# Performance work log

Measured on AMD Instinct MI355X. Metric: run time of the kernel, lower is better.

## Reference

```python
import jax, jax.numpy as jnp
import numpy as np

B, T, DIM = 4, 2048, 2048
H = 16
Q_LORA, KV_LORA = 1536, 512
ROPE_D, NOPE_D, V_D = 64, 128, 128
Q_HEAD_D = NOPE_D + ROPE_D  # 192
EPS = 1e-6
ROPE_THETA = 500000.0


def rmsnorm(x, w):
    xf = x.astype(jnp.float32)
    rms = jax.lax.rsqrt(jnp.mean(xf * xf, axis=-1, keepdims=True) + EPS)
    return (xf * rms).astype(x.dtype) * w


def apply_rope(x, cos, sin):
    # x: (B,T,H,d); cos/sin: (T,d//2). Complex mult on interleaved pairs.
    d = x.shape[-1]
    xp = x.reshape(*x.shape[:-1], d // 2, 2)
    x0, x1 = xp[..., 0], xp[..., 1]
    c = cos[None, :, None, :]
    s = sin[None, :, None, :]
    o0 = x0 * c - x1 * s
    o1 = x0 * s + x1 * c
    return jnp.stack([o0, o1], axis=-1).reshape(x.shape)


def setup_inputs() -> dict:
    key = jax.random.key(0)
    ks = jax.random.split(key, 8)
    x = jax.random.normal(ks[0], (B, T, DIM), dtype=jnp.float32)
    # RoPE freqs as in standard precompute_freqs_cis
    inv_freq = 1.0 / (ROPE_THETA ** (np.arange(0, ROPE_D, 2, dtype=np.float32) / ROPE_D))
    t = np.arange(T, dtype=np.float32)
    ang = np.outer(t, inv_freq)  # (T, 32)
    freqs_cos = jnp.asarray(np.cos(ang))
    freqs_sin = jnp.asarray(np.sin(ang))
    # causal additive mask (1,1,T,T)
    mask = jnp.where(jnp.tril(jnp.ones((T, T), dtype=bool)), 0.0, -1e9).astype(jnp.float32)[None, None]
    sc = lambda fan_in: 1.0 / np.sqrt(fan_in)
    q_down_w = jax.random.normal(ks[1], (Q_LORA, DIM), dtype=jnp.float32) * sc(DIM)
    q_norm_w = jnp.ones((Q_LORA,), dtype=jnp.float32)
    q_up_nope_w = jax.random.normal(ks[2], (H * NOPE_D, Q_LORA), dtype=jnp.float32) * sc(Q_LORA)
    q_up_rope_w = jax.random.normal(ks[3], (H * ROPE_D, Q_LORA), dtype=jnp.float32) * sc(Q_LORA)
    kv_down_w = jax.random.normal(ks[4], (KV_LORA + ROPE_D, DIM), dtype=jnp.float32) * sc(DIM)
    kv_norm_w = jnp.ones((KV_LORA,), dtype=jnp.float32)
    kv_up_w = jax.random.normal(ks[5], (H * (NOPE_D + V_D), KV_LORA), dtype=jnp.float32) * sc(KV_LORA)
    wo_w = jax.random.normal(ks[6], (DIM, H * V_D), dtype=jnp.float32) * sc(H * V_D)
    return {"x": x, "freqs_cos": freqs_cos, "freqs_sin": freqs_sin, "mask": mask,
            "q_down_w": q_down_w, "q_norm_w": q_norm_w, "q_up_nope_w": q_up_nope_w,
            "q_up_rope_w": q_up_rope_w, "kv_down_w": kv_down_w, "kv_norm_w": kv_norm_w,
            "kv_up_w": kv_up_w, "wo_w": wo_w}


def reference(x, freqs_cos, freqs_sin, mask, q_down_w, q_norm_w, q_up_nope_w,
              q_up_rope_w, kv_down_w, kv_norm_w, kv_up_w, wo_w):
    b, t, _ = x.shape
    # Q path: low-rank down -> RMSNorm -> nope/rope up projections
    c_q = rmsnorm(x @ q_down_w.T, q_norm_w)                      # (B,T,q_lora)
    q_nope = (c_q @ q_up_nope_w.T).reshape(b, t, H, NOPE_D)
    q_rope = (c_q @ q_up_rope_w.T).reshape(b, t, H, ROPE_D)
    q_rope = apply_rope(q_rope, freqs_cos, freqs_sin)
    q = jnp.concatenate([q_nope, q_rope], axis=-1)               # (B,T,H,192)
    # KV path: shared low-rank latent + per-sequence rope key
    kv_raw = x @ kv_down_w.T                                     # (B,T,512+64)
    c_kv = kv_raw[..., :KV_LORA]
    k_rope = kv_raw[..., KV_LORA:][:, :, None, :]                # (B,T,1,64)
    k_rope = apply_rope(k_rope, freqs_cos, freqs_sin)
    k_rope = jnp.broadcast_to(k_rope, (b, t, H, ROPE_D))
    kv = (rmsnorm(c_kv, kv_norm_w) @ kv_up_w.T).reshape(b, t, H, NOPE_D + V_D)
    k_nope = kv[..., :NOPE_D]
    v = kv[..., NOPE_D:]                                         # (B,T,H,128)
    k = jnp.concatenate([k_nope, k_rope], axis=-1)               # (B,T,H,192)
    scale = Q_HEAD_D ** -0.5
    attn = jnp.einsum('bthd,bshd->bhts', q, k) * scale + mask    # (B,H,T,T)
    attn = jax.nn.softmax(attn, axis=-1)
    out = jnp.einsum('bhts,bshd->bthd', attn, v).reshape(b, t, H * V_D)
    return out @ wo_w.T
```

## Files before the change

kernel.cpp:

```cpp
#include <hip/hip_runtime.h>

#define BB 4
#define TT 2048
#define HH 16
#define ROWS (BB*TT)

typedef unsigned short u16;
typedef __bf16 bf16x8 __attribute__((ext_vector_type(8)));
typedef float f32x4 __attribute__((ext_vector_type(4)));
typedef u16 u16x8 __attribute__((ext_vector_type(8)));
typedef u16 u16x4 __attribute__((ext_vector_type(4)));

__device__ __forceinline__ u16 f2bf(float f) {
  unsigned u = __float_as_uint(f);
  u += 0x7fffu + ((u >> 16) & 1u);
  return (u16)(u >> 16);
}
__device__ __forceinline__ float bf2f(u16 h) {
  return __uint_as_float(((unsigned)h) << 16);
}

__device__ __forceinline__ void gload_lds16(const u16* g, u16* l) {
  __builtin_amdgcn_global_load_lds((const __attribute__((address_space(1))) void*)g,
                                   (__attribute__((address_space(3))) void*)l, 16, 0, 0);
}

__global__ __launch_bounds__(256) void cast_all(const float* __restrict__ x,
                                                const float* __restrict__ qdw,
                                                const float* __restrict__ kvdw,
                                                const float* __restrict__ qunw,
                                                const float* __restrict__ qurw,
                                                const float* __restrict__ kvuw,
                                                const float* __restrict__ wow,
                                                u16* __restrict__ xb,
                                                u16* __restrict__ wdc,
                                                u16* __restrict__ wuc,
                                                u16* __restrict__ wkvu,
                                                u16* __restrict__ wwo,
                                                float qsc) {
  const long s0 = 1536L*2048, s1 = 768L*2048, s2 = 2048L*1536,
             s3 = 1024L*1536, s4 = 4096L*512,  s5 = 2048L*2048,
             s6 = (long)ROWS*2048;
  const long total = s0+s1+s2+s3+s4+s5+s6;
  long i = ((long)blockIdx.x * 256 + threadIdx.x) * 4;
  long stride = (long)gridDim.x * 1024;
  for (; i < total; i += stride) {
    long off = i; const float* src; u16* dst; float sc = 1.f; long lim = -1;
    if (off < s0)               { src = qdw;  dst = wdc; }
    else if ((off -= s0) < s1)  { src = kvdw; dst = wdc + s0; lim = 576L*2048; }
    else if ((off -= s1) < s2)  { src = qunw; dst = wuc; sc = qsc; }
    else if ((off -= s2) < s3)  { src = qurw; dst = wuc + s2; }
    else if ((off -= s3) < s4)  { src = kvuw; dst = wkvu; }
    else if ((off -= s4) < s5)  { src = wow;  dst = wwo; }
    else { off -= s5;             src = x;    dst = xb; }
    u16x4 o;
    if (lim < 0 || off + 3 < lim) {
      float4 v = *(const float4*)(src + off);
      o = (u16x4){ f2bf(v.x*sc), f2bf(v.y*sc), f2bf(v.z*sc), f2bf(v.w*sc) };
    } else {
#pragma unroll
      for (int e = 0; e < 4; ++e) o[e] = (off + e < lim) ? f2bf(src[off+e]*sc) : (u16)0;
    }
    *(u16x4*)(dst + off) = o;
  }
}


template<int MODE>
__global__ __launch_bounds__(512, 2) void gemm256(const u16* __restrict__ A,
                                                  const u16* __restrict__ Bm,
                                                  void* __restrict__ Cv,
                                                  int M, int N, int K, int lda) {
  __shared__ __align__(16) u16 lds[32768];
  const int tid = threadIdx.x;
  const int lane = tid & 63, wid = tid >> 6;
  const int wm = (wid >> 2) * 128;
  const int wn = (wid & 3) * 64;

  const int nx = gridDim.x;
  int id = blockIdx.y * nx + blockIdx.x;
  const int cpx = (nx * gridDim.y) >> 3;
  id = (id & 7) * cpx + (id >> 3);
  const int m0 = (id / nx) * 256;
  const int n0 = (id % nx) * 256;

  const int NT = K >> 5;

  f32x4 acc[8][4] = {};

  auto stage = [&](int kt, int d) {
#pragma unroll
    for (int j = 0; j < 2; ++j) {
      int c = j*512 + tid;
      int row = c >> 2;
      int colb = (c & 3) << 4;
      int srcb = colb ^ (((row >> 1) & 3) << 4);
      const u16* ga = (const u16*)((const char*)A + ((long)(m0 + row) * lda + kt*32) * 2 + srcb);
      gload_lds16(ga, (u16*)((char*)lds + d*32768 + c*16));
      const u16* gb = (const u16*)((const char*)Bm + ((long)(n0 + row) * K + kt*32) * 2 + srcb);
      gload_lds16(gb, (u16*)((char*)lds + d*32768 + 16384 + c*16));
    }
  };

  stage(0, 0);
  stage(1, 1);

  const int lr = lane & 15;
  const int kb = (lane >> 4) << 4;

  for (int kt = 0; kt < NT; ++kt) {
    const int cur = kt & 1;
    if (kt + 1 < NT) asm volatile("s_waitcnt vmcnt(4)" ::: "memory");
    else             asm volatile("s_waitcnt vmcnt(0)" ::: "memory");
    __builtin_amdgcn_s_barrier();
    __builtin_amdgcn_sched_barrier(0);

    const char* Ab = (const char*)lds + cur*32768;
    const char* Bb = Ab + 16384;
    bf16x8 af[8], bf[4];
#pragma unroll
    for (int i = 0; i < 8; ++i) {
      int r = wm + i*16 + lr;
      af[i] = *(const bf16x8*)(Ab + r*64 + (kb ^ (((r >> 1) & 3) << 4)));
    }
#pragma unroll
    for (int i = 0; i < 4; ++i) {
      int r = wn + i*16 + lr;
      bf[i] = *(const bf16x8*)(Bb + r*64 + (kb ^ (((r >> 1) & 3) << 4)));
    }
    __builtin_amdgcn_s_setprio(1);
#pragma unroll
    for (int i = 0; i < 8; ++i)
#pragma unroll
      for (int j = 0; j < 4; ++j)
        acc[i][j] = __builtin_amdgcn_mfma_f32_16x16x32_bf16(af[i], bf[j], acc[i][j], 0, 0, 0);
    __builtin_amdgcn_s_setprio(0);
    __builtin_amdgcn_sched_barrier(0);
    __builtin_amdgcn_s_barrier();
    if (kt + 2 < NT) stage(kt + 2, cur);
  }

  const int orow = (lane >> 4) << 2;
  const int ocol = lane & 15;
#pragma unroll
  for (int mf = 0; mf < 8; ++mf)
#pragma unroll
    for (int nf = 0; nf < 4; ++nf) {
      long rbase = (long)(m0 + wm + mf*16 + orow);
      int col = n0 + wn + nf*16 + ocol;
      if (MODE == 0) {
#pragma unroll
        for (int rr = 0; rr < 4; ++rr)
          ((float*)Cv)[(rbase + rr) * (long)N + col] = acc[mf][nf][rr];
      } else {
#pragma unroll
        for (int rr = 0; rr < 4; ++rr)
          ((u16*)Cv)[(rbase + rr) * (long)N + col] = f2bf(acc[mf][nf][rr]);
      }
    }
}

__global__ __launch_bounds__(512, 2) void gemm_up(const u16* __restrict__ dk,
                                                  const u16* __restrict__ wuc,
                                                  const u16* __restrict__ wkvu,
                                                  u16* __restrict__ qcat,
                                                  u16* __restrict__ kn,
                                                  u16* __restrict__ Vt) {
  __shared__ __align__(16) u16 lds[32768];
  const int tid = threadIdx.x;
  const int lane = tid & 63, wid = tid >> 6;
  const int wm = (wid >> 2) * 128;
  const int wn = (wid & 3) * 64;

  const int bid = blockIdx.x;
  const bool isQ = bid < 384;
  int lid = isQ ? bid : bid - 384;
  const int nwg = isQ ? 384 : 512;
  const int nx  = isQ ? 12 : 16;
  const int cpx = nwg >> 3;
  lid = (lid & 7) * cpx + (lid >> 3);
  const int m0 = (lid / nx) * 256;
  const int n0 = (lid % nx) * 256;

  const u16* A  = isQ ? dk : (dk + 1536);
  const u16* Bm = isQ ? wuc : wkvu;
  const int K   = isQ ? 1536 : 512;
  const int lda = 2304;
  const int NT  = K >> 5;

  f32x4 acc[8][4] = {};

  auto stage = [&](int kt, int d) {
#pragma unroll
    for (int j = 0; j < 2; ++j) {
      int c = j*512 + tid;
      int row = c >> 2;
      int colb = (c & 3) << 4;
      int srcb = colb ^ (((row >> 1) & 3) << 4);
      const u16* ga = (const u16*)((const char*)A + ((long)(m0 + row) * lda + kt*32) * 2 + srcb);
      gload_lds16(ga, (u16*)((char*)lds + d*32768 + c*16));
      const u16* gb = (const u16*)((const char*)Bm + ((long)(n0 + row) * K + kt*32) * 2 + srcb);
      gload_lds16(gb, (u16*)((char*)lds + d*32768 + 16384 + c*16));
    }
  };

  stage(0, 0);
  stage(1, 1);

  const int lr = lane & 15;
  const int kb = (lane >> 4) << 4;

  for (int kt = 0; kt < NT; ++kt) {
    const int cur = kt & 1;
    if (kt + 1 < NT) asm volatile("s_waitcnt vmcnt(4)" ::: "memory");
    else             asm volatile("s_waitcnt vmcnt(0)" ::: "memory");
    __builtin_amdgcn_s_barrier();
    __builtin_amdgcn_sched_barrier(0);

    const char* Ab = (const char*)lds + cur*32768;
    const char* Bb = Ab + 16384;
    bf16x8 af[8], bf[4];
#pragma unroll
    for (int i = 0; i < 8; ++i) {
      int r = wm + i*16 + lr;
      af[i] = *(const bf16x8*)(Ab + r*64 + (kb ^ (((r >> 1) & 3) << 4)));
    }
#pragma unroll
    for (int i = 0; i < 4; ++i) {
      int r = wn + i*16 + lr;
      bf[i] = *(const bf16x8*)(Bb + r*64 + (kb ^ (((r >> 1) & 3) << 4)));
    }
    __builtin_amdgcn_s_setprio(1);
#pragma unroll
    for (int i = 0; i < 8; ++i)
#pragma unroll
      for (int j = 0; j < 4; ++j)
        acc[i][j] = __builtin_amdgcn_mfma_f32_16x16x32_bf16(af[i], bf[j], acc[i][j], 0, 0, 0);
    __builtin_amdgcn_s_setprio(0);
    __builtin_amdgcn_sched_barrier(0);
    __builtin_amdgcn_s_barrier();
    if (kt + 2 < NT) stage(kt + 2, cur);
  }

  const int orow = (lane >> 4) << 2;
  const int ocol = lane & 15;
#pragma unroll
  for (int mf = 0; mf < 8; ++mf)
#pragma unroll
    for (int nf = 0; nf < 4; ++nf) {
      long rbase = (long)(m0 + wm + mf*16 + orow);
      int col = n0 + wn + nf*16 + ocol;
      if (isQ) {
#pragma unroll
        for (int rr = 0; rr < 4; ++rr)
          qcat[(rbase + rr) * 3072L + col] = f2bf(acc[mf][nf][rr]);
      } else {
        int h = col >> 8, inner = col & 255;
        if (inner < 128) {
#pragma unroll
          for (int rr = 0; rr < 4; ++rr)
            kn[(rbase + rr) * 2048L + h*128 + inner] = f2bf(acc[mf][nf][rr]);
        } else {
          int bb = (int)(rbase >> 11);
          int t  = (int)(rbase & 2047);
          long vo = ((long)(bb*16 + h) * 128 + (inner - 128)) * 2048 + t;
          u16x4 o = { f2bf(acc[mf][nf][0]), f2bf(acc[mf][nf][1]),
                      f2bf(acc[mf][nf][2]), f2bf(acc[mf][nf][3]) };
          *(u16x4*)(Vt + vo) = o;
        }
      }
    }
}

__global__ __launch_bounds__(256) void rms_rope_dk(u16* __restrict__ dk,
                                                   const float* __restrict__ qnw,
                                                   const float* __restrict__ kvnw,
                                                   u16* __restrict__ Kr,
                                                   const float* __restrict__ cosb,
                                                   const float* __restrict__ sinb) {
  const long row = blockIdx.x;
  u16* x = dk + row * 2304;
  const int i = threadIdx.x * 8;
  float sq = 0.f, sk = 0.f;
  u16x8 v = *(const u16x8*)(x + i);
  {
    float s = 0.f;
#pragma unroll
    for (int e = 0; e < 8; ++e) { float f = bf2f(v[e]); s += f*f; }
    if (i < 1536) sq = s; else sk = s;
  }
#pragma unroll
  for (int off = 32; off > 0; off >>= 1) {
    sq += __shfl_down(sq, off);
    sk += __shfl_down(sk, off);
  }
  __shared__ float redq[4], redk[4];
  if ((threadIdx.x & 63) == 0) {
    redq[threadIdx.x >> 6] = sq;
    redk[threadIdx.x >> 6] = sk;
  }
  __syncthreads();
  float rq = rsqrtf((redq[0]+redq[1]+redq[2]+redq[3]) * (1.f/1536.f) + 1e-6f);
  float rk = rsqrtf((redk[0]+redk[1]+redk[2]+redk[3]) * (1.f/512.f) + 1e-6f);
  {
    float r = (i < 1536) ? rq : rk;
    const float* w = (i < 1536) ? (qnw + i) : (kvnw + (i - 1536));
    u16x8 o;
#pragma unroll
    for (int e = 0; e < 8; ++e) o[e] = f2bf(bf2f(v[e]) * r * w[e]);
    *(u16x8*)(x + i) = o;
  }
  if (threadIdx.x < 32) {
    const int t = (int)(row & (TT-1));
    int ii = threadIdx.x;
    float x0 = bf2f(x[2048 + 2*ii]);
    float x1 = bf2f(x[2048 + 2*ii + 1]);
    float c = cosb[t*32 + ii], s = sinb[t*32 + ii];
    Kr[row*64 + 2*ii]     = f2bf(x0*c - x1*s);
    Kr[row*64 + 2*ii + 1] = f2bf(x0*s + x1*c);
  }
}

__global__ __launch_bounds__(512) void flash_attn10(const u16* __restrict__ qcat,
                                                    const u16* __restrict__ kn,
                                                    const u16* __restrict__ kr,
                                                    const u16* __restrict__ Vt,
                                                    const float* __restrict__ cosb,
                                                    const float* __restrict__ sinb,
                                                    u16* __restrict__ O) {
  __shared__ __align__(16) u16 lds[36864];
  const int bid = blockIdx.x;
  const int u = bid & 255, sl = bid >> 8;
  const int a = u >> 6;
  const int bh = u & 63;
  const int qt = sl ? a : (7 - a);
  const int b = bh >> 4, h = bh & 15;
  const int wid = threadIdx.x >> 6, lane = threadIdx.x & 63;
  const int q0 = qt*256 + wid*32;
  const long browq = (long)b * TT + q0;
  const long browk = (long)b * TT;
  const int l16 = lane >> 4;
  const int l8  = lane >> 3;
  const int lx16   = (lane & 15) * 16;
  const int lx8_16 = (lane & 7) * 16;
  const int co = l16 * 16;
  const float QSCE = 0.10411754661f;

  bf16x8 qf[2][6];
#pragma unroll
  for (int f = 0; f < 2; ++f) {
    long row = browq + f*16 + (lane & 15);
#pragma unroll
    for (int ks = 0; ks < 4; ++ks)
      qf[f][ks] = *(const bf16x8*)(qcat + row * 3072 + h*128 + ks*32 + l16 * 8);
    const int t = (int)(row & (TT-1));
#pragma unroll
    for (int ks = 0; ks < 2; ++ks) {
      bf16x8 v = *(const bf16x8*)(qcat + row * 3072 + 2048 + h*64 + ks*32 + l16 * 8);
      const int ib = ks*16 + l16*4;
#pragma unroll
      for (int pp = 0; pp < 4; ++pp) {
        float x0 = (float)v[2*pp], x1 = (float)v[2*pp+1];
        float c = cosb[t*32 + ib + pp], s = sinb[t*32 + ib + pp];
        v[2*pp]   = (__bf16)((x0*c - x1*s) * QSCE);
        v[2*pp+1] = (__bf16)((x0*s + x1*c) * QSCE);
      }
      qf[f][4+ks] = v;
    }
  }

  bf16x8 vones;
#pragma unroll
  for (int e = 0; e < 8; ++e) vones[e] = (__bf16)1.0f;

  f32x4 oacc[2][8] = {};
  f32x4 lsum[2] = {};

  u16* pw = lds + 20480 + wid * 2048;

  const int nIter = 4*qt + 4;
  for (int it = 0; it < nIter; ++it) {
    const int s0 = it * 64;
#pragma unroll
    for (int j = 0; j < 2; ++j) {
      int c = j*8 + wid;
      int r = c*4 + l16;
      int cb = lx16 ^ ((r & 7) << 4);
      const u16* src = (const u16*)((const char*)kn + (browk + s0 + r) * 4096 + h * 256 + cb);
      gload_lds16(src, lds + c*512);
    }
    {
      int c = wid;
      int r = c*8 + l8;
      int cb = lx8_16 ^ ((r & 7) << 4);
      const u16* src = (const u16*)((const char*)kr + (browk + s0 + r) * 128 + cb);
      gload_lds16(src, lds + 8192 + c*512);
    }
#pragma unroll
    for (int j = 0; j < 2; ++j) {
      int c = j*8 + wid;
      int d = c*8 + l8;
      int cb = lx8_16 ^ ((d & 7) << 4);
      const u16* src = (const u16*)((const char*)Vt + ((long)bh*128 + d) * (TT*2) + (long)s0*2 + cb);
      gload_lds16(src, lds + 12288 + c*512);
    }
    __syncthreads();

    const bool skip0 = s0 > q0 + 15;
    const bool skip1 = s0 > q0 + 31;
    if (!skip0 || !skip1) {
      __builtin_amdgcn_s_setprio(1);
      f32x4 sacc[2][4] = {};
#pragma unroll
      for (int nt = 0; nt < 4; ++nt) {
        const int r = nt*16 + (lane & 15);
        const int swz = (r & 7) << 4;
        bf16x8 kf[6];
#pragma unroll
        for (int ks = 0; ks < 4; ++ks)
          kf[ks] = *(const bf16x8*)((const char*)lds + r*256 + ((ks*64 + co) ^ swz));
#pragma unroll
        for (int ks = 0; ks < 2; ++ks)
          kf[4+ks] = *(const bf16x8*)((const char*)lds + 16384 + r*128 + ((ks*64 + co) ^ swz));
        if (!skip0) {
#pragma unroll
          for (int ks = 0; ks < 6; ++ks)
            sacc[0][nt] = __builtin_amdgcn_mfma_f32_16x16x32_bf16(qf[0][ks], kf[ks], sacc[0][nt], 0, 0, 0);
        }
        if (!skip1) {
#pragma unroll
          for (int ks = 0; ks < 6; ++ks)
            sacc[1][nt] = __builtin_amdgcn_mfma_f32_16x16x32_bf16(qf[1][ks], kf[ks], sacc[1][nt], 0, 0, 0);
        }
      }
#pragma unroll
      for (int f = 0; f < 2; ++f) {
        const bool skipf = f ? skip1 : skip0;
        if (skipf) continue;
        const int qmin = q0 + f*16;
        const int qb = qmin + (l16 << 2);
        if (s0 + 63 > qmin) {
#pragma unroll
          for (int nt = 0; nt < 4; ++nt) {
            int sc = s0 + nt*16 + (lane & 15);
#pragma unroll
            for (int rr = 0; rr < 4; ++rr)
              if (sc > qb + rr) sacc[f][nt][rr] = -1e30f;
          }
        }
        const int lb2 = (lane & 15) * 2;
#pragma unroll
        for (int rr = 0; rr < 4; ++rr) {
          float p0 = exp2f(sacc[f][0][rr] - 16.f);
          float p1 = exp2f(sacc[f][1][rr] - 16.f);
          float p2 = exp2f(sacc[f][2][rr] - 16.f);
          float p3 = exp2f(sacc[f][3][rr] - 16.f);
          const int prow = f*16 + (l16 << 2) + rr;
          const int sw = (prow & 7) << 4;
          char* pb = (char*)pw + prow*128;
          *(u16*)(pb + ((     lb2) ^ sw)) = f2bf(p0);
          *(u16*)(pb + (( 32 + lb2) ^ sw)) = f2bf(p1);
          *(u16*)(pb + (( 64 + lb2) ^ sw)) = f2bf(p2);
          *(u16*)(pb + (( 96 + lb2) ^ sw)) = f2bf(p3);
        }
      }
#pragma unroll
      for (int ks = 0; ks < 2; ++ks) {
        const int cb = ks*64 + co;
        bf16x8 vf[8];
#pragma unroll
        for (int vt = 0; vt < 8; ++vt) {
          int row = vt*16 + (lane & 15);
          vf[vt] = *(const bf16x8*)((const char*)lds + 24576 + row*128 + (cb ^ ((row & 7) << 4)));
        }
#pragma unroll
        for (int f = 0; f < 2; ++f) {
          if (f ? skip1 : skip0) continue;
          int prow = f*16 + (lane & 15);
          bf16x8 pa = *(const bf16x8*)((const char*)pw + prow*128 + (cb ^ ((prow & 7) << 4)));
          lsum[f] = __builtin_amdgcn_mfma_f32_16x16x32_bf16(pa, vones, lsum[f], 0, 0, 0);
#pragma unroll
          for (int vt = 0; vt < 8; ++vt)
            oacc[f][vt] = __builtin_amdgcn_mfma_f32_16x16x32_bf16(pa, vf[vt], oacc[f][vt], 0, 0, 0);
        }
      }
      __builtin_amdgcn_s_setprio(0);
    }
    __syncthreads();
  }

#pragma unroll
  for (int f = 0; f < 2; ++f) {
    float inv[4];
#pragma unroll
    for (int rr = 0; rr < 4; ++rr) inv[rr] = 1.f / lsum[f][rr];
#pragma unroll
    for (int vt = 0; vt < 8; ++vt)
#pragma unroll
      for (int rr = 0; rr < 4; ++rr) {
        long row = browq + f*16 + (l16 << 2) + rr;
        int col = h*128 + vt*16 + (lane & 15);
        O[row * 2048 + col] = f2bf(oacc[f][vt][rr] * inv[rr]);
      }
  }
}

static inline long minl(long a, long b) { return a < b ? a : b; }

extern "C" void kernel_launch(void* const* d_in, const int* in_sizes, int n_in,
                              void* d_out, int out_size, void* d_ws, size_t ws_size,
                              hipStream_t stream) {
  const float* x    = (const float*)d_in[0];
  const float* fcos = (const float*)d_in[1];
  const float* fsin = (const float*)d_in[2];
  const float* qdw  = (const float*)d_in[4];
  const float* qnw  = (const float*)d_in[5];
  const float* qunw = (const float*)d_in[6];
  const float* qurw = (const float*)d_in[7];
  const float* kvdw = (const float*)d_in[8];
  const float* kvnw = (const float*)d_in[9];
  const float* kvuw = (const float*)d_in[10];
  const float* wow  = (const float*)d_in[11];
  float* out = (float*)d_out;

  char* p = (char*)d_ws;
  auto alloc = [&](size_t bytes) { char* r = p; p += (bytes + 255) & ~(size_t)255; return r; };

  u16* xb   = (u16*)alloc((size_t)ROWS*2048*2);
  u16* wdc  = (u16*)alloc((size_t)2304*2048*2);
  u16* wuc  = (u16*)alloc((size_t)3072*1536*2);
  u16* wkvu = (u16*)alloc((size_t)4096*512*2);
  u16* wwo  = (u16*)alloc((size_t)2048*2048*2);
  u16* dk   = (u16*)alloc((size_t)ROWS*2304*2);
  u16* qcat = (u16*)alloc((size_t)ROWS*3072*2);
  u16* kn   = (u16*)alloc((size_t)ROWS*2048*2);
  u16* Vt   = (u16*)alloc((size_t)ROWS*2048*2);
  u16* kro  = (u16*)alloc((size_t)ROWS*64*2);

  u16* Ob = xb;

  const float QSC_E = 0.10411754661f;

  cast_all<<<4096, 256, 0, stream>>>(x, qdw, kvdw, qunw, qurw, kvuw, wow,
                                     xb, wdc, wuc, wkvu, wwo, QSC_E);

  gemm256<1><<<dim3(9, 32), 512, 0, stream>>>(xb, wdc, dk, ROWS, 2304, 2048, 2048);
  rms_rope_dk<<<ROWS, 256, 0, stream>>>(dk, qnw, kvnw, kro, fcos, fsin);
  gemm_up<<<896, 512, 0, stream>>>(dk, wuc, wkvu, qcat, kn, Vt);
  flash_attn10<<<512, 512, 0, stream>>>(qcat, kn, kro, Vt, fcos, fsin, Ob);
  gemm256<0><<<dim3(8, 32), 512, 0, stream>>>(Ob, wwo, out, ROWS, 2048, 2048, 2048);
}
```

Baseline: 515.8 us.

## Split-K the down-projection GEMM and fuse the partial-sum reduction into RMSNorm

The down-projection GEMM (8192x2304x2048) now runs as a split-K kernel. Its 288 tiles become 576 blocks, each covering half of K, and each half writes bf16 partial results to a separate buffer; the second buffer reuses the qcat workspace. The RMSNorm/RoPE kernel adds the two partials before normalizing, so no separate reduction pass is needed. This is meant to fill the GPU's compute units better with one 288-tile wave. In exchange it doubles the output writes and reads, and rounds each partial sum to bf16 before the sum is taken.

New measurement: 503.1 us (median of 2 runs). 2.5% less time.

```diff
diff --git a/kernel.cpp b/kernel.cpp
--- a/kernel.cpp
+++ b/kernel.cpp
@@ -65,7 +65,6 @@
   }
 }
 
-
 template<int MODE>
 __global__ __launch_bounds__(512, 2) void gemm256(const u16* __restrict__ A,
                                                   const u16* __restrict__ Bm,
@@ -157,6 +156,94 @@
         for (int rr = 0; rr < 4; ++rr)
           ((u16*)Cv)[(rbase + rr) * (long)N + col] = f2bf(acc[mf][nf][rr]);
       }
+    }
+}
+
+__global__ __launch_bounds__(512, 2) void gemm_down(const u16* __restrict__ A,
+                                                    const u16* __restrict__ Bm,
+                                                    u16* __restrict__ dkA,
+                                                    u16* __restrict__ dkB) {
+  __shared__ __align__(16) u16 lds[32768];
+  const int tid = threadIdx.x;
+  const int lane = tid & 63, wid = tid >> 6;
+  const int wm = (wid >> 2) * 128;
+  const int wn = (wid & 3) * 64;
+
+  int id = blockIdx.y * 9 + blockIdx.x;
+  id = (id & 7) * 72 + (id >> 3);
+  const int rrow = id / 9;
+  const int n0 = (id % 9) * 256;
+  const int m0 = (rrow >> 1) * 256;
+  const int kpart = rrow & 1;
+  const int k0 = kpart * 1024;
+  u16* Cv = kpart ? dkB : dkA;
+  const int NT = 32;
+
+  f32x4 acc[8][4] = {};
+
+  auto stage = [&](int kt, int d) {
+#pragma unroll
+    for (int j = 0; j < 2; ++j) {
+      int c = j*512 + tid;
+      int row = c >> 2;
+      int colb = (c & 3) << 4;
+      int srcb = colb ^ (((row >> 1) & 3) << 4);
+      const u16* ga = (const u16*)((const char*)A + ((long)(m0 + row) * 2048 + k0 + kt*32) * 2 + srcb);
+      gload_lds16(ga, (u16*)((char*)lds + d*32768 + c*16));
+      const u16* gb = (const u16*)((const char*)Bm + ((long)(n0 + row) * 2048 + k0 + kt*32) * 2 + srcb);
+      gload_lds16(gb, (u16*)((char*)lds + d*32768 + 16384 + c*16));
+    }
+  };
+
+  stage(0, 0);
+  stage(1, 1);
+
+  const int lr = lane & 15;
+  const int kb = (lane >> 4) << 4;
+
+  for (int kt = 0; kt < NT; ++kt) {
+    const int cur = kt & 1;
+    if (kt + 1 < NT) asm volatile("s_waitcnt vmcnt(4)" ::: "memory");
+    else             asm volatile("s_waitcnt vmcnt(0)" ::: "memory");
+    __builtin_amdgcn_s_barrier();
+    __builtin_amdgcn_sched_barrier(0);
+
+    const char* Ab = (const char*)lds + cur*32768;
+    const char* Bb = Ab + 16384;
+    bf16x8 af[8], bf[4];
+#pragma unroll
+    for (int i = 0; i < 8; ++i) {
+      int r = wm + i*16 + lr;
+      af[i] = *(const bf16x8*)(Ab + r*64 + (kb ^ (((r >> 1) & 3) << 4)));
+    }
+#pragma unroll
+    for (int i = 0; i < 4; ++i) {
+      int r = wn + i*16 + lr;
+      bf[i] = *(const bf16x8*)(Bb + r*64 + (kb ^ (((r >> 1) & 3) << 4)));
+    }
+    __builtin_amdgcn_s_setprio(1);
+#pragma unroll
+    for (int i = 0; i < 8; ++i)
+#pragma unroll
+      for (int j = 0; j < 4; ++j)
+        acc[i][j] = __builtin_amdgcn_mfma_f32_16x16x32_bf16(af[i], bf[j], acc[i][j], 0, 0, 0);
+    __builtin_amdgcn_s_setprio(0);
+    __builtin_amdgcn_sched_barrier(0);
+    __builtin_amdgcn_s_barrier();
+    if (kt + 2 < NT) stage(kt + 2, cur);
+  }
+
+  const int orow = (lane >> 4) << 2;
+  const int ocol = lane & 15;
+#pragma unroll
+  for (int mf = 0; mf < 8; ++mf)
+#pragma unroll
+    for (int nf = 0; nf < 4; ++nf) {
+      long rbase = (long)(m0 + wm + mf*16 + orow);
+      int col = n0 + wn + nf*16 + ocol;
+#pragma unroll
+      for (int rr = 0; rr < 4; ++rr)
+        Cv[(rbase + rr) * 2304L + col] = f2bf(acc[mf][nf][rr]);
     }
 }
 
@@ -272,21 +359,25 @@
     }
 }
 
-__global__ __launch_bounds__(256) void rms_rope_dk(u16* __restrict__ dk,
+__global__ __launch_bounds__(256) void rms_rope_dk(u16* __restrict__ dkA,
+                                                   const u16* __restrict__ dkB,
                                                    const float* __restrict__ qnw,
                                                    const float* __restrict__ kvnw,
                                                    u16* __restrict__ Kr,
                                                    const float* __restrict__ cosb,
                                                    const float* __restrict__ sinb) {
   const long row = blockIdx.x;
-  u16* x = dk + row * 2304;
+  u16* xa = dkA + row * 2304;
+  const u16* xb2 = dkB + row * 2304;
   const int i = threadIdx.x * 8;
   float sq = 0.f, sk = 0.f;
-  u16x8 v = *(const u16x8*)(x + i);
+  u16x8 v1 = *(const u16x8*)(xa + i);
+  u16x8 v2 = *(const u16x8*)(xb2 + i);
+  float fv[8];
   {
     float s = 0.f;
 #pragma unroll
-    for (int e = 0; e < 8; ++e) { float f = bf2f(v[e]); s += f*f; }
+    for (int e = 0; e < 8; ++e) { fv[e] = bf2f(v1[e]) + bf2f(v2[e]); s += fv[e]*fv[e]; }
     if (i < 1536) sq = s; else sk = s;
   }
 #pragma unroll
@@ -307,14 +398,14 @@
     const float* w = (i < 1536) ? (qnw + i) : (kvnw + (i - 1536));
     u16x8 o;
 #pragma unroll
-    for (int e = 0; e < 8; ++e) o[e] = f2bf(bf2f(v[e]) * r * w[e]);
-    *(u16x8*)(x + i) = o;
+    for (int e = 0; e < 8; ++e) o[e] = f2bf(fv[e] * r * w[e]);
+    *(u16x8*)(xa + i) = o;
   }
   if (threadIdx.x < 32) {
     const int t = (int)(row & (TT-1));
     int ii = threadIdx.x;
-    float x0 = bf2f(x[2048 + 2*ii]);
-    float x1 = bf2f(x[2048 + 2*ii + 1]);
+    float x0 = bf2f(xa[2048 + 2*ii])     + bf2f(xb2[2048 + 2*ii]);
+    float x1 = bf2f(xa[2048 + 2*ii + 1]) + bf2f(xb2[2048 + 2*ii + 1]);
     float c = cosb[t*32 + ii], s = sinb[t*32 + ii];
     Kr[row*64 + 2*ii]     = f2bf(x0*c - x1*s);
     Kr[row*64 + 2*ii + 1] = f2bf(x0*s + x1*c);
@@ -537,15 +628,16 @@
   u16* Vt   = (u16*)alloc((size_t)ROWS*2048*2);
   u16* kro  = (u16*)alloc((size_t)ROWS*64*2);
 
-  u16* Ob = xb;
+  u16* Ob  = xb;
+  u16* dk2 = qcat;
 
   const float QSC_E = 0.10411754661f;
 
   cast_all<<<4096, 256, 0, stream>>>(x, qdw, kvdw, qunw, qurw, kvuw, wow,
                                      xb, wdc, wuc, wkvu, wwo, QSC_E);
 
-  gemm256<1><<<dim3(9, 32), 512, 0, stream>>>(xb, wdc, dk, ROWS, 2304, 2048, 2048);
-  rms_rope_dk<<<ROWS, 256, 0, stream>>>(dk, qnw, kvnw, kro, fcos, fsin);
+  gemm_down<<<dim3(9, 64), 512, 0, stream>>>(xb, wdc, dk, dk2);
+  rms_rope_dk<<<ROWS, 256, 0, stream>>>(dk, dk2, qnw, kvnw, kro, fcos, fsin);
   gemm_up<<<896, 512, 0, stream>>>(dk, wuc, wkvu, qcat, kn, Vt);
   flash_attn10<<<512, 512, 0, stream>>>(qcat, kn, kro, Vt, fcos, fsin, Ob);
   gemm256<0><<<dim3(8, 32), 512, 0, stream>>>(Ob, wwo, out, ROWS, 2048, 2048, 2048);
```
